# Performance work log

Hardware: AMD Instinct MI355X
Metric: run time of the kernel (lower is better)

## Reference

```python
import jax, jax.numpy as jnp
import numpy as np

B, N, K, DIN, C = 2, 20480, 16, 32, 64  # C = 2*d_out
EPS = 1e-5


def _ln(x, g, b):
    m = jnp.mean(x, axis=-1, keepdims=True)
    v = jnp.mean((x - m) ** 2, axis=-1, keepdims=True)
    return (x - m) * jax.lax.rsqrt(v + EPS) * g + b


def _gather(pc, idx):
    # pc: (B, N, D), idx: (B, N, K) -> (B, N, K, D)
    Bq, Nq, Kq = idx.shape
    D = pc.shape[-1]
    flat = idx.reshape(Bq, Nq * Kq, 1)
    return jnp.take_along_axis(pc, flat, axis=1).reshape(Bq, Nq, Kq, D)


def setup_inputs() -> dict:
    key = jax.random.key(0)
    ks = jax.random.split(key, 40)
    rn = lambda k, s, sc=0.05: jax.random.normal(k, s, dtype=jnp.float32) * sc
    inp = {
        "feature": rn(ks[0], (B, DIN, N, 1), 1.0),
        "xyz": jax.random.uniform(ks[1], (B, N, 3), dtype=jnp.float32),
        "W1": rn(ks[2], (C, DIN)), "b1": rn(ks[3], (C,)),
        "Wq": rn(ks[4], (C, C)), "bq": rn(ks[5], (C,)),
        "Wk": rn(ks[6], (C, C)), "bk": rn(ks[7], (C,)),
        "Wv": rn(ks[8], (C, C)), "bv": rn(ks[9], (C,)),
        "Wd1": rn(ks[10], (3, 3), 0.3), "bd1": rn(ks[11], (3,)),
        "lnd1_g": 1.0 + rn(ks[12], (3,)), "lnd1_b": rn(ks[13], (3,)),
        "Wd2": rn(ks[14], (C, 3), 0.3), "bd2": rn(ks[15], (C,)),
        "Wg1": rn(ks[16], (C, C)), "bg1": rn(ks[17], (C,)),
        "lng1_g": 1.0 + rn(ks[18], (C,)), "lng1_b": rn(ks[19], (C,)),
        "Wg2": rn(ks[20], (C, C)), "bg2": rn(ks[21], (C,)),
        "lng2_g": 1.0 + rn(ks[22], (C,)), "lng2_b": rn(ks[23], (C,)),
        "Wmlp": rn(ks[24], (C, C)),
        "bnm_g": 1.0 + rn(ks[25], (C,)), "bnm_b": rn(ks[26], (C,)),
        "bnm_m": rn(ks[27], (C,)), "bnm_v": 1.0 + jax.random.uniform(ks[28], (C,), dtype=jnp.float32) * 0.1,
        "Wsc": rn(ks[29], (C, DIN)),
        "bns_g": 1.0 + rn(ks[30], (C,)), "bns_b": rn(ks[31], (C,)),
        "bns_m": rn(ks[32], (C,)), "bns_v": 1.0 + jax.random.uniform(ks[33], (C,), dtype=jnp.float32) * 0.1,
        "neigh_idx": jax.random.randint(ks[34], (B, N, K), 0, N),
    }
    return inp


def reference(feature, xyz, W1, b1, Wq, bq, Wk, bk, Wv, bv, Wd1, bd1, lnd1_g, lnd1_b,
              Wd2, bd2, Wg1, bg1, lng1_g, lng1_b, Wg2, bg2, lng2_g, lng2_b,
              Wmlp, bnm_g, bnm_b, bnm_m, bnm_v, Wsc, bns_g, bns_b, bns_m, bns_v,
              neigh_idx):
    f = jnp.transpose(feature[..., 0], (0, 2, 1))          # (B, N, DIN)
    x = f @ W1.T + b1                                      # (B, N, C)
    q = x @ Wq.T + bq                                      # (B, N, C)
    kf = _gather(x @ Wk.T + bk, neigh_idx)                 # (B, N, K, C)
    vf = _gather(x @ Wv.T + bv, neigh_idx)                 # (B, N, K, C)
    knn_xyz = _gather(xyz, neigh_idx)                      # (B, N, K, 3)
    rel = xyz[:, :, None, :] - knn_xyz                     # (B, N, K, 3)
    pos = rel @ Wd1.T + bd1
    pos = jax.nn.relu(_ln(pos, lnd1_g, lnd1_b))
    pos = pos @ Wd2.T + bd2                                # (B, N, K, C)
    attn = q[:, :, None, :] - kf + pos
    attn = jax.nn.relu(_ln(attn, lng1_g, lng1_b)) @ Wg1.T + bg1
    attn = jax.nn.relu(_ln(attn, lng2_g, lng2_b)) @ Wg2.T + bg2
    attn = jax.nn.softmax(attn, axis=2)                    # softmax over K
    res = jnp.sum(attn * (vf + pos), axis=2)               # (B, N, C)
    # mlp: 1x1 conv (no bias) + BN(eval) + ReLU
    res = res @ Wmlp.T
    res = jax.nn.relu(bnm_g * (res - bnm_m) * jax.lax.rsqrt(bnm_v + EPS) + bnm_b)
    # shortcut: 1x1 conv (no bias) + BN(eval) + ReLU
    sc = f @ Wsc.T
    sc = jax.nn.relu(bns_g * (sc - bns_m) * jax.lax.rsqrt(bns_v + EPS) + bns_b)
    out = jax.nn.leaky_relu(res + sc, negative_slope=0.2)  # (B, N, C)
    return jnp.transpose(out, (0, 2, 1))[..., None]        # (B, C, N, 1)
```

## Files before the change

### kernel.cpp

```cpp
#include <hip/hip_runtime.h>

#define N_ 20480
#define EPS_ 1e-5f

typedef __bf16 bf16;
typedef __attribute__((ext_vector_type(8))) __bf16 bf16x8;
typedef __attribute__((ext_vector_type(4))) float f32x4;
typedef __attribute__((ext_vector_type(2))) float f32x2;

#define WS_WG1   0
#define WS_WG2   8192
#define WS_PCST  16384
#define WS_L1    17408
#define WS_L2    17920
#define WS_BG1   18432
#define WS_BG2   18688
#define WS_WQ    18944
#define WS_WK    23040
#define WS_WV    27136
#define WS_WSC   31232
#define WS_WMLP  35328
#define WS_BQ    43520
#define WS_BK    43776
#define WS_BV    44032
#define WS_BSC   44288
#define WS_BMLP  44544
#define WS_PD1   44800
#define WS_FLAG  44872
#define WS_PREP  45056

template <typename T>
__device__ __forceinline__ float ldf(const T* p, size_t i) { return (float)p[i]; }

__global__ void detect_dtype(const unsigned int* __restrict__ xyz_raw, int* __restrict__ flag) {
  __shared__ int cnt[256];
  int t = threadIdx.x;
  int local = 0;
  for (int i = t; i < 4096; i += 256) {
    unsigned int wv = xyz_raw[i];
    unsigned int b1 = (wv >> 8) & 0xFFu;
    local += (b1 >= 0x30u && b1 < 0x45u) ? 1 : 0;
  }
  cnt[t] = local;
  __syncthreads();
  for (int s = 128; s > 0; s >>= 1) {
    if (t < s) cnt[t] += cnt[t + s];
    __syncthreads();
  }
  if (t == 0) flag[0] = (cnt[0] > 2048) ? 1 : 0;
}

template <typename T>
__device__ void prep_body(const T* W1, const T* b1, const T* Wq, const T* bq,
                          const T* Wk, const T* bk, const T* Wv, const T* bv,
                          const T* Wd1, const T* bd1, const T* lnd1_g, const T* lnd1_b,
                          const T* Wd2, const T* bd2,
                          const T* Wg1, const T* bg1, const T* lng1_g, const T* lng1_b,
                          const T* Wg2, const T* bg2, const T* lng2_g, const T* lng2_b,
                          const T* Wmlp, const T* bnm_g, const T* bnm_b, const T* bnm_m, const T* bnm_v,
                          const T* Wsc, const T* bns_g, const T* bns_b, const T* bns_m, const T* bns_v,
                          char* wsp) {
  const int t = threadIdx.x;
  bf16* wg1bf = (bf16*)(wsp + WS_WG1);
  bf16* wg2bf = (bf16*)(wsp + WS_WG2);
  bf16* wmlpbf = (bf16*)(wsp + WS_WMLP);
  bf16* wscbf = (bf16*)(wsp + WS_WSC);
  bf16* wqbf = (bf16*)(wsp + WS_WQ);
  bf16* wkbf = (bf16*)(wsp + WS_WK);
  bf16* wvbf = (bf16*)(wsp + WS_WV);
  float* pcst = (float*)(wsp + WS_PCST);
  float* l1c = (float*)(wsp + WS_L1);
  float* l2c = (float*)(wsp + WS_L2);
  float* bg1f = (float*)(wsp + WS_BG1);
  float* bg2f = (float*)(wsp + WS_BG2);
  float* bqf = (float*)(wsp + WS_BQ);
  float* bkf = (float*)(wsp + WS_BK);
  float* bvf = (float*)(wsp + WS_BV);
  float* bscf = (float*)(wsp + WS_BSC);
  float* bmlpf = (float*)(wsp + WS_BMLP);
  float* pd1 = (float*)(wsp + WS_PD1);

  for (int i = t; i < 4096; i += 256) {
    wg1bf[i] = (__bf16)ldf(Wg1, i);
    wg2bf[i] = (__bf16)ldf(Wg2, i);
    int c = i >> 6;
    float s = ldf(bnm_g, c) * rsqrtf(ldf(bnm_v, c) + EPS_);
    wmlpbf[i] = (__bf16)(s * ldf(Wmlp, i));
  }
  for (int i = t; i < 2048; i += 256) {
    int c = i >> 5;
    float s = ldf(bns_g, c) * rsqrtf(ldf(bns_v, c) + EPS_);
    wscbf[i] = (__bf16)(s * ldf(Wsc, i));
  }
  for (int o = t; o < 2048; o += 256) {
    int c = o >> 5, d = o & 31;
    float aq = 0.f, ak = 0.f, av = 0.f;
    for (int cc = 0; cc < 64; ++cc) {
      float w1v = ldf(W1, cc * 32 + d);
      aq = fmaf(ldf(Wq, c * 64 + cc), w1v, aq);
      ak = fmaf(ldf(Wk, c * 64 + cc), w1v, ak);
      av = fmaf(ldf(Wv, c * 64 + cc), w1v, av);
    }
    wqbf[o] = (__bf16)aq; wkbf[o] = (__bf16)ak; wvbf[o] = (__bf16)av;
  }
  if (t < 64) {
    pcst[t * 4 + 0] = ldf(Wd2, t * 3 + 0);
    pcst[t * 4 + 1] = ldf(Wd2, t * 3 + 1);
    pcst[t * 4 + 2] = ldf(Wd2, t * 3 + 2);
    pcst[t * 4 + 3] = ldf(bd2, t);
    l1c[t * 2 + 0] = ldf(lng1_g, t); l1c[t * 2 + 1] = ldf(lng1_b, t);
    l2c[t * 2 + 0] = ldf(lng2_g, t); l2c[t * 2 + 1] = ldf(lng2_b, t);
    bg1f[t] = ldf(bg1, t); bg2f[t] = ldf(bg2, t);
    float aq = ldf(bq, t), ak = ldf(bk, t), av = ldf(bv, t);
    for (int cc = 0; cc < 64; ++cc) {
      float b1v = ldf(b1, cc);
      aq = fmaf(ldf(Wq, t * 64 + cc), b1v, aq);
      ak = fmaf(ldf(Wk, t * 64 + cc), b1v, ak);
      av = fmaf(ldf(Wv, t * 64 + cc), b1v, av);
    }
    bqf[t] = aq; bkf[t] = ak; bvf[t] = av;
    float sm = ldf(bnm_g, t) * rsqrtf(ldf(bnm_v, t) + EPS_);
    bmlpf[t] = ldf(bnm_b, t) - ldf(bnm_m, t) * sm;
    float ss = ldf(bns_g, t) * rsqrtf(ldf(bns_v, t) + EPS_);
    bscf[t] = ldf(bns_b, t) - ldf(bns_m, t) * ss;
  }
  if (t < 9) pd1[t] = ldf(Wd1, t);
  if (t < 3) {
    pd1[9 + t] = ldf(bd1, t);
    pd1[12 + t] = ldf(lnd1_g, t);
    pd1[15 + t] = ldf(lnd1_b, t);
  }
}

__launch_bounds__(256)
__global__ void prep_kernel(const void* W1, const void* b1, const void* Wq, const void* bq,
                            const void* Wk, const void* bk, const void* Wv, const void* bv,
                            const void* Wd1, const void* bd1, const void* lnd1_g, const void* lnd1_b,
                            const void* Wd2, const void* bd2,
                            const void* Wg1, const void* bg1, const void* lng1_g, const void* lng1_b,
                            const void* Wg2, const void* bg2, const void* lng2_g, const void* lng2_b,
                            const void* Wmlp, const void* bnm_g, const void* bnm_b, const void* bnm_m,
                            const void* bnm_v, const void* Wsc, const void* bns_g, const void* bns_b,
                            const void* bns_m, const void* bns_v, char* wsp) {
  const int* flag = (const int*)(wsp + WS_FLAG);
  if (flag[0])
    prep_body<bf16>((const bf16*)W1, (const bf16*)b1, (const bf16*)Wq, (const bf16*)bq,
                    (const bf16*)Wk, (const bf16*)bk, (const bf16*)Wv, (const bf16*)bv,
                    (const bf16*)Wd1, (const bf16*)bd1, (const bf16*)lnd1_g, (const bf16*)lnd1_b,
                    (const bf16*)Wd2, (const bf16*)bd2,
                    (const bf16*)Wg1, (const bf16*)bg1, (const bf16*)lng1_g, (const bf16*)lng1_b,
                    (const bf16*)Wg2, (const bf16*)bg2, (const bf16*)lng2_g, (const bf16*)lng2_b,
                    (const bf16*)Wmlp, (const bf16*)bnm_g, (const bf16*)bnm_b, (const bf16*)bnm_m,
                    (const bf16*)bnm_v, (const bf16*)Wsc, (const bf16*)bns_g, (const bf16*)bns_b,
                    (const bf16*)bns_m, (const bf16*)bns_v, wsp);
  else
    prep_body<float>((const float*)W1, (const float*)b1, (const float*)Wq, (const float*)bq,
                     (const float*)Wk, (const float*)bk, (const float*)Wv, (const float*)bv,
                     (const float*)Wd1, (const float*)bd1, (const float*)lnd1_g, (const float*)lnd1_b,
                     (const float*)Wd2, (const float*)bd2,
                     (const float*)Wg1, (const float*)bg1, (const float*)lng1_g, (const float*)lng1_b,
                     (const float*)Wg2, (const float*)bg2, (const float*)lng2_g, (const float*)lng2_b,
                     (const float*)Wmlp, (const float*)bnm_g, (const float*)bnm_b, (const float*)bnm_m,
                     (const float*)bnm_v, (const float*)Wsc, (const float*)bns_g, (const float*)bns_b,
                     (const float*)bns_m, (const float*)bns_v, wsp);
}

template <typename T>
__device__ void xqkv_body(const T* feat, const char* wsp,
                          bf16* q_ws, bf16* k_ws, bf16* v_ws, float (*tile)[68]) {
  const int t = threadIdx.x, w = t >> 6, lane = t & 63;
  const int m = lane & 15, g = lane >> 4;
  const int p0 = blockIdx.x * 64 + w * 16;
  const int b = p0 / N_, n0 = p0 % N_;
  const bf16* wqbf = (const bf16*)(wsp + WS_WQ);
  const bf16* wkbf = (const bf16*)(wsp + WS_WK);
  const bf16* wvbf = (const bf16*)(wsp + WS_WV);
  const float* bqf = (const float*)(wsp + WS_BQ);
  const float* bkf = (const float*)(wsp + WS_BK);
  const float* bvf = (const float*)(wsp + WS_BV);
  float (*tw)[68] = tile + w * 16;

  bf16x8 fa;
  #pragma unroll
  for (int j = 0; j < 8; ++j)
    fa[j] = (__bf16)ldf(feat, ((size_t)b * 32 + g * 8 + j) * N_ + n0 + m);

  auto matmul16 = [&](const bf16* wbf, const float* bias, float* ob) {
    #pragma unroll
    for (int tt = 0; tt < 4; ++tt) {
      bf16x8 wf = *(const bf16x8*)(wbf + (tt * 16 + m) * 32 + g * 8);
      float bb = bias[tt * 16 + m];
      f32x4 ci = {bb, bb, bb, bb};
      ci = __builtin_amdgcn_mfma_f32_16x16x32_bf16(fa, wf, ci, 0, 0, 0);
      #pragma unroll
      for (int r = 0; r < 4; ++r) tw[g * 4 + r][tt * 16 + m] = ci[r];
    }
    #pragma unroll
    for (int s = 0; s < 2; ++s) {
      f32x4 v0 = *(f32x4*)&tw[m][s * 32 + g * 8];
      f32x4 v1 = *(f32x4*)&tw[m][s * 32 + g * 8 + 4];
      #pragma unroll
      for (int r = 0; r < 4; ++r) { ob[s * 8 + r] = v0[r]; ob[s * 8 + 4 + r] = v1[r]; }
    }
  };
  float ob[16];
  bf16x8 o0, o1;
  matmul16(wqbf, bqf, ob);
  #pragma unroll
  for (int j = 0; j < 8; ++j) { o0[j] = (__bf16)ob[j]; o1[j] = (__bf16)ob[8 + j]; }
  *(bf16x8*)(q_ws + (size_t)(p0 + m) * 64 + g * 8) = o0;
  *(bf16x8*)(q_ws + (size_t)(p0 + m) * 64 + 32 + g * 8) = o1;
  matmul16(wkbf, bkf, ob);
  #pragma unroll
  for (int j = 0; j < 8; ++j) { o0[j] = (__bf16)ob[j]; o1[j] = (__bf16)ob[8 + j]; }
  *(bf16x8*)(k_ws + (size_t)(p0 + m) * 64 + g * 8) = o0;
  *(bf16x8*)(k_ws + (size_t)(p0 + m) * 64 + 32 + g * 8) = o1;
  matmul16(wvbf, bvf, ob);
  #pragma unroll
  for (int j = 0; j < 8; ++j) { o0[j] = (__bf16)ob[j]; o1[j] = (__bf16)ob[8 + j]; }
  *(bf16x8*)(v_ws + (size_t)(p0 + m) * 64 + g * 8) = o0;
  *(bf16x8*)(v_ws + (size_t)(p0 + m) * 64 + 32 + g * 8) = o1;
}

__launch_bounds__(256)
__global__ void xqkv_kernel(const void* feat, char* wsp,
                            bf16* q_ws, bf16* k_ws, bf16* v_ws) {
  __shared__ float tile[64][68];
  const int* flag = (const int*)(wsp + WS_FLAG);
  if (flag[0]) xqkv_body<bf16>((const bf16*)feat, wsp, q_ws, k_ws, v_ws, tile);
  else         xqkv_body<float>((const float*)feat, wsp, q_ws, k_ws, v_ws, tile);
}

template <typename T>
__device__ void attn_body(const T* xyz, const int* nidx, const char* wsp,
                          bf16* qres, const bf16* k_ws, const bf16* v_ws,
                          f32x4* pcstL, f32x2* l1L, f32x2* l2L,
                          float (*vpf)[68], float (*scr)[68]) {
  const int t = threadIdx.x;
  ((float*)pcstL)[t] = ((const float*)(wsp + WS_PCST))[t];
  if (t < 128) ((float*)l1L)[t] = ((const float*)(wsp + WS_L1))[t];
  else if (t < 256) ((float*)l2L)[t - 128] = ((const float*)(wsp + WS_L2))[t - 128];
  __syncthreads();

  const int w = t >> 6, lane = t & 63, m = lane & 15, g = lane >> 4;
  const int p = blockIdx.x * 4 + w;
  const int b = p / N_;
  float (*vw)[68] = vpf + w * 16;
  float (*sw)[68] = scr + w * 16;

  const float* pd1 = (const float*)(wsp + WS_PD1);
  const float* bg1f = (const float*)(wsp + WS_BG1);
  const float* bg2f = (const float*)(wsp + WS_BG2);
  const bf16* wg1bf = (const bf16*)(wsp + WS_WG1);
  const bf16* wg2bf = (const bf16*)(wsp + WS_WG2);

  float bg1r[4], bg2r[4];
  #pragma unroll
  for (int tt = 0; tt < 4; ++tt) { bg1r[tt] = bg1f[tt * 16 + m]; bg2r[tt] = bg2f[tt * 16 + m]; }

  float xp = ldf(xyz, (size_t)p * 3 + 0);
  float yp = ldf(xyz, (size_t)p * 3 + 1);
  float zp = ldf(xyz, (size_t)p * 3 + 2);

  int idx = nidx[(size_t)p * 16 + m];
  size_t pg = (size_t)b * N_ + idx;
  bf16x8 kf0 = *(const bf16x8*)(k_ws + pg * 64 + g * 8);
  bf16x8 kf1 = *(const bf16x8*)(k_ws + pg * 64 + 32 + g * 8);
  bf16x8 vf0 = *(const bf16x8*)(v_ws + pg * 64 + g * 8);
  bf16x8 vf1 = *(const bf16x8*)(v_ws + pg * 64 + 32 + g * 8);
  bf16x8 qf0 = *(const bf16x8*)(qres + (size_t)p * 64 + g * 8);
  bf16x8 qf1 = *(const bf16x8*)(qres + (size_t)p * 64 + 32 + g * 8);
  float nx = ldf(xyz, pg * 3 + 0), ny = ldf(xyz, pg * 3 + 1), nz = ldf(xyz, pg * 3 + 2);

  float rx = xp - nx, ry = yp - ny, rz = zp - nz;
  float pp0 = pd1[0] * rx + pd1[1] * ry + pd1[2] * rz + pd1[9];
  float pp1 = pd1[3] * rx + pd1[4] * ry + pd1[5] * rz + pd1[10];
  float pp2 = pd1[6] * rx + pd1[7] * ry + pd1[8] * rz + pd1[11];
  float mu3 = (pp0 + pp1 + pp2) * (1.f / 3.f);
  float q0 = pp0 - mu3, q1 = pp1 - mu3, q2 = pp2 - mu3;
  float vr3 = (q0 * q0 + q1 * q1 + q2 * q2) * (1.f / 3.f);
  float rs3 = rsqrtf(vr3 + EPS_);
  float h0 = fmaxf(q0 * rs3 * pd1[12] + pd1[15], 0.f);
  float h1 = fmaxf(q1 * rs3 * pd1[13] + pd1[16], 0.f);
  float h2 = fmaxf(q2 * rs3 * pd1[14] + pd1[17], 0.f);

  float a[16];
  #pragma unroll
  for (int s = 0; s < 2; ++s)
    #pragma unroll
    for (int half = 0; half < 2; ++half) {
      f32x4 vout;
      #pragma unroll
      for (int q4 = 0; q4 < 4; ++q4) {
        int j = half * 4 + q4;
        int c = s * 32 + g * 8 + j;
        f32x4 pc = pcstL[c];
        float pos = fmaf(h0, pc[0], fmaf(h1, pc[1], fmaf(h2, pc[2], pc[3])));
        float kv = (float)((s == 0) ? kf0[j] : kf1[j]);
        float vv = (float)((s == 0) ? vf0[j] : vf1[j]);
        float qv = (float)((s == 0) ? qf0[j] : qf1[j]);
        vout[q4] = vv + pos;
        a[s * 8 + j] = qv - kv + pos;
      }
      *(f32x4*)&vw[m][s * 32 + g * 8 + half * 4] = vout;
    }

  f32x4 acc[4];
  bf16x8 hf0, hf1;

  {
    float s1 = 0.f, s2 = 0.f;
    #pragma unroll
    for (int i = 0; i < 16; ++i) { s1 += a[i]; s2 = fmaf(a[i], a[i], s2); }
    s1 += __shfl_xor(s1, 16); s2 += __shfl_xor(s2, 16);
    s1 += __shfl_xor(s1, 32); s2 += __shfl_xor(s2, 32);
    float mean = s1 * (1.f / 64.f);
    float var = s2 * (1.f / 64.f) - mean * mean;
    float rsv = rsqrtf(var + EPS_);
    #pragma unroll
    for (int s = 0; s < 2; ++s)
      #pragma unroll
      for (int j = 0; j < 8; ++j) {
        int c = s * 32 + g * 8 + j;
        f32x2 lc = l1L[c];
        float hh = fmaxf(fmaf((a[s * 8 + j] - mean) * rsv, lc[0], lc[1]), 0.f);
        if (s == 0) hf0[j] = (__bf16)hh; else hf1[j] = (__bf16)hh;
      }
  }
  #pragma unroll
  for (int tt = 0; tt < 4; ++tt) {
    bf16x8 w0 = *(const bf16x8*)(wg1bf + (tt * 16 + m) * 64 + g * 8);
    bf16x8 w1 = *(const bf16x8*)(wg1bf + (tt * 16 + m) * 64 + 32 + g * 8);
    f32x4 ci = {bg1r[tt], bg1r[tt], bg1r[tt], bg1r[tt]};
    ci = __builtin_amdgcn_mfma_f32_16x16x32_bf16(hf0, w0, ci, 0, 0, 0);
    ci = __builtin_amdgcn_mfma_f32_16x16x32_bf16(hf1, w1, ci, 0, 0, 0);
    acc[tt] = ci;
  }
  #pragma unroll
  for (int tt = 0; tt < 4; ++tt)
    #pragma unroll
    for (int r = 0; r < 4; ++r)
      sw[g * 4 + r][tt * 16 + m] = acc[tt][r];
  #pragma unroll
  for (int s = 0; s < 2; ++s) {
    f32x4 v0 = *(f32x4*)&sw[m][s * 32 + g * 8];
    f32x4 v1 = *(f32x4*)&sw[m][s * 32 + g * 8 + 4];
    #pragma unroll
    for (int r = 0; r < 4; ++r) { a[s * 8 + r] = v0[r]; a[s * 8 + 4 + r] = v1[r]; }
  }
  {
    float s1 = 0.f, s2 = 0.f;
    #pragma unroll
    for (int i = 0; i < 16; ++i) { s1 += a[i]; s2 = fmaf(a[i], a[i], s2); }
    s1 += __shfl_xor(s1, 16); s2 += __shfl_xor(s2, 16);
    s1 += __shfl_xor(s1, 32); s2 += __shfl_xor(s2, 32);
    float mean = s1 * (1.f / 64.f);
    float var = s2 * (1.f / 64.f) - mean * mean;
    float rsv = rsqrtf(var + EPS_);
    #pragma unroll
    for (int s = 0; s < 2; ++s)
      #pragma unroll
      for (int j = 0; j < 8; ++j) {
        int c = s * 32 + g * 8 + j;
        f32x2 lc = l2L[c];
        float hh = fmaxf(fmaf((a[s * 8 + j] - mean) * rsv, lc[0], lc[1]), 0.f);
        if (s == 0) hf0[j] = (__bf16)hh; else hf1[j] = (__bf16)hh;
      }
  }
  #pragma unroll
  for (int tt = 0; tt < 4; ++tt) {
    bf16x8 w0 = *(const bf16x8*)(wg2bf + (tt * 16 + m) * 64 + g * 8);
    bf16x8 w1 = *(const bf16x8*)(wg2bf + (tt * 16 + m) * 64 + 32 + g * 8);
    f32x4 ci = {bg2r[tt], bg2r[tt], bg2r[tt], bg2r[tt]};
    ci = __builtin_amdgcn_mfma_f32_16x16x32_bf16(hf0, w0, ci, 0, 0, 0);
    ci = __builtin_amdgcn_mfma_f32_16x16x32_bf16(hf1, w1, ci, 0, 0, 0);
    acc[tt] = ci;
  }
  float resv[4];
  #pragma unroll
  for (int tt = 0; tt < 4; ++tt) {
    f32x4 l = acc[tt];
    float mx = fmaxf(fmaxf(l[0], l[1]), fmaxf(l[2], l[3]));
    mx = fmaxf(mx, __shfl_xor(mx, 16));
    mx = fmaxf(mx, __shfl_xor(mx, 32));
    float x0 = __expf(l[0] - mx), x1 = __expf(l[1] - mx);
    float x2 = __expf(l[2] - mx), x3 = __expf(l[3] - mx);
    float ss = x0 + x1 + x2 + x3;
    ss += __shfl_xor(ss, 16); ss += __shfl_xor(ss, 32);
    int cc = tt * 16 + m;
    float part = x0 * vw[g * 4 + 0][cc] + x1 * vw[g * 4 + 1][cc]
               + x2 * vw[g * 4 + 2][cc] + x3 * vw[g * 4 + 3][cc];
    part += __shfl_xor(part, 16); part += __shfl_xor(part, 32);
    resv[tt] = part / ss;
  }
  float outv = (g == 0) ? resv[0] : (g == 1) ? resv[1] : (g == 2) ? resv[2] : resv[3];
  qres[(size_t)p * 64 + lane] = (__bf16)outv;
}

__launch_bounds__(256)
__global__ void attn_kernel(const void* xyz, const int* __restrict__ nidx, char* wsp,
                            bf16* qres, const bf16* k_ws, const bf16* v_ws) {
  __shared__ f32x4 pcstL[64];
  __shared__ f32x2 l1L[64];
  __shared__ f32x2 l2L[64];
  __shared__ float vpf[64][68];
  __shared__ float scr[64][68];
  const int* flag = (const int*)(wsp + WS_FLAG);
  if (flag[0])
    attn_body<bf16>((const bf16*)xyz, nidx, wsp, qres, k_ws, v_ws, pcstL, l1L, l2L, vpf, scr);
  else
    attn_body<float>((const float*)xyz, nidx, wsp, qres, k_ws, v_ws, pcstL, l1L, l2L, vpf, scr);
}

template <typename T>
__device__ void out_body(const T* feat, const bf16* res_ws, const char* wsp, T* out,
                         float (*tileT)[68]) {
  const int t = threadIdx.x, w = t >> 6, lane = t & 63;
  const int m = lane & 15, g = lane >> 4;
  const int p0blk = blockIdx.x * 64;
  const int b = p0blk / N_, n0 = p0blk % N_;
  const int p0w = p0blk + w * 16;
  const bf16* wmlpbf = (const bf16*)(wsp + WS_WMLP);
  const bf16* wscbf = (const bf16*)(wsp + WS_WSC);
  const float* bmlpf = (const float*)(wsp + WS_BMLP);
  const float* bscf = (const float*)(wsp + WS_BSC);

  bf16x8 ar0 = *(const bf16x8*)(res_ws + (size_t)(p0w + m) * 64 + g * 8);
  bf16x8 ar1 = *(const bf16x8*)(res_ws + (size_t)(p0w + m) * 64 + 32 + g * 8);
  bf16x8 af;
  #pragma unroll
  for (int j = 0; j < 8; ++j)
    af[j] = (__bf16)ldf(feat, ((size_t)b * 32 + g * 8 + j) * N_ + (n0 + w * 16) + m);

  #pragma unroll
  for (int tt = 0; tt < 4; ++tt) {
    bf16x8 wm0 = *(const bf16x8*)(wmlpbf + (tt * 16 + m) * 64 + g * 8);
    bf16x8 wm1 = *(const bf16x8*)(wmlpbf + (tt * 16 + m) * 64 + 32 + g * 8);
    bf16x8 wsf = *(const bf16x8*)(wscbf + (tt * 16 + m) * 32 + g * 8);
    float bm = bmlpf[tt * 16 + m], bs = bscf[tt * 16 + m];
    f32x4 cm = {bm, bm, bm, bm};
    cm = __builtin_amdgcn_mfma_f32_16x16x32_bf16(ar0, wm0, cm, 0, 0, 0);
    cm = __builtin_amdgcn_mfma_f32_16x16x32_bf16(ar1, wm1, cm, 0, 0, 0);
    f32x4 cs = {bs, bs, bs, bs};
    cs = __builtin_amdgcn_mfma_f32_16x16x32_bf16(af, wsf, cs, 0, 0, 0);
    #pragma unroll
    for (int r = 0; r < 4; ++r) {
      float o = fmaxf(cm[r], 0.f) + fmaxf(cs[r], 0.f);
      o = (o > 0.f) ? o : 0.2f * o;
      tileT[tt * 16 + m][w * 16 + g * 4 + r] = o;
    }
  }
  __syncthreads();
  const int ln = t & 63, grp = t >> 6;
  #pragma unroll
  for (int k = 0; k < 16; ++k) {
    int c2 = grp * 16 + k;
    out[((size_t)b * 64 + c2) * N_ + n0 + ln] = (T)tileT[c2][ln];
  }
}

__launch_bounds__(256)
__global__ void out_kernel(const void* feat, const bf16* res_ws, char* wsp, void* out) {
  __shared__ float tileT[64][68];
  const int* flag = (const int*)(wsp + WS_FLAG);
  if (flag[0]) out_body<bf16>((const bf16*)feat, res_ws, wsp, (bf16*)out, tileT);
  else         out_body<float>((const float*)feat, res_ws, wsp, (float*)out, tileT);
}

extern "C" void kernel_launch(void* const* d_in, const int* in_sizes, int n_in,
                              void* d_out, int out_size, void* d_ws, size_t ws_size,
                              hipStream_t stream) {
  const void* feature = d_in[0];
  const void* xyz     = d_in[1];
  const int*  nidx    = (const int*)d_in[34];

  char* ws = (char*)d_ws;
  bf16* q_ws = (bf16*)(ws + WS_PREP);
  bf16* k_ws = (bf16*)(ws + WS_PREP + 5242880);
  bf16* v_ws = (bf16*)(ws + WS_PREP + 10485760);

  detect_dtype<<<1, 256, 0, stream>>>((const unsigned int*)xyz, (int*)(ws + WS_FLAG));
  prep_kernel<<<1, 256, 0, stream>>>(d_in[2], d_in[3], d_in[4], d_in[5], d_in[6], d_in[7],
                                     d_in[8], d_in[9], d_in[10], d_in[11], d_in[12], d_in[13],
                                     d_in[14], d_in[15], d_in[16], d_in[17], d_in[18], d_in[19],
                                     d_in[20], d_in[21], d_in[22], d_in[23], d_in[24], d_in[25],
                                     d_in[26], d_in[27], d_in[28], d_in[29], d_in[30], d_in[31],
                                     d_in[32], d_in[33], ws);
  xqkv_kernel<<<640, 256, 0, stream>>>(feature, ws, q_ws, k_ws, v_ws);
  attn_kernel<<<10240, 256, 0, stream>>>(xyz, nidx, ws, q_ws, k_ws, v_ws);
  out_kernel<<<640, 256, 0, stream>>>(feature, q_ws, ws, d_out);
}
```

Measured before the change: 293.9 us.

## Store attention LDS scratch in bf16, raise occupancy hint, parallelize prep kernel

```diff
diff --git a/kernel.cpp b/kernel.cpp
--- a/kernel.cpp
+++ b/kernel.cpp
@@ -5,6 +5,7 @@
 
 typedef __bf16 bf16;
 typedef __attribute__((ext_vector_type(8))) __bf16 bf16x8;
+typedef __attribute__((ext_vector_type(4))) __bf16 bf16x4;
 typedef __attribute__((ext_vector_type(4))) float f32x4;
 typedef __attribute__((ext_vector_type(2))) float f32x2;
 
@@ -60,7 +61,8 @@
                           const T* Wmlp, const T* bnm_g, const T* bnm_b, const T* bnm_m, const T* bnm_v,
                           const T* Wsc, const T* bns_g, const T* bns_b, const T* bns_m, const T* bns_v,
                           char* wsp) {
-  const int t = threadIdx.x;
+  const int tid = blockIdx.x * 256 + threadIdx.x;
+  const int T_ = gridDim.x * 256;
   bf16* wg1bf = (bf16*)(wsp + WS_WG1);
   bf16* wg2bf = (bf16*)(wsp + WS_WG2);
   bf16* wmlpbf = (bf16*)(wsp + WS_WMLP);
@@ -80,19 +82,19 @@
   float* bmlpf = (float*)(wsp + WS_BMLP);
   float* pd1 = (float*)(wsp + WS_PD1);
 
-  for (int i = t; i < 4096; i += 256) {
+  for (int i = tid; i < 4096; i += T_) {
     wg1bf[i] = (__bf16)ldf(Wg1, i);
     wg2bf[i] = (__bf16)ldf(Wg2, i);
     int c = i >> 6;
     float s = ldf(bnm_g, c) * rsqrtf(ldf(bnm_v, c) + EPS_);
     wmlpbf[i] = (__bf16)(s * ldf(Wmlp, i));
   }
-  for (int i = t; i < 2048; i += 256) {
+  for (int i = tid; i < 2048; i += T_) {
     int c = i >> 5;
     float s = ldf(bns_g, c) * rsqrtf(ldf(bns_v, c) + EPS_);
     wscbf[i] = (__bf16)(s * ldf(Wsc, i));
   }
-  for (int o = t; o < 2048; o += 256) {
+  for (int o = tid; o < 2048; o += T_) {
     int c = o >> 5, d = o & 31;
     float aq = 0.f, ak = 0.f, av = 0.f;
     for (int cc = 0; cc < 64; ++cc) {
@@ -103,7 +105,8 @@
     }
     wqbf[o] = (__bf16)aq; wkbf[o] = (__bf16)ak; wvbf[o] = (__bf16)av;
   }
-  if (t < 64) {
+  if (tid < 64) {
+    int t = tid;
     pcst[t * 4 + 0] = ldf(Wd2, t * 3 + 0);
     pcst[t * 4 + 1] = ldf(Wd2, t * 3 + 1);
     pcst[t * 4 + 2] = ldf(Wd2, t * 3 + 2);
@@ -124,11 +127,12 @@
     float ss = ldf(bns_g, t) * rsqrtf(ldf(bns_v, t) + EPS_);
     bscf[t] = ldf(bns_b, t) - ldf(bns_m, t) * ss;
   }
-  if (t < 9) pd1[t] = ldf(Wd1, t);
-  if (t < 3) {
-    pd1[9 + t] = ldf(bd1, t);
-    pd1[12 + t] = ldf(lnd1_g, t);
-    pd1[15 + t] = ldf(lnd1_b, t);
+  if (tid >= 64 && tid < 64 + 9) pd1[tid - 64] = ldf(Wd1, tid - 64);
+  if (tid >= 80 && tid < 83) {
+    int i = tid - 80;
+    pd1[9 + i] = ldf(bd1, i);
+    pd1[12 + i] = ldf(lnd1_g, i);
+    pd1[15 + i] = ldf(lnd1_b, i);
   }
 }
 
@@ -235,7 +239,7 @@
 __device__ void attn_body(const T* xyz, const int* nidx, const char* wsp,
                           bf16* qres, const bf16* k_ws, const bf16* v_ws,
                           f32x4* pcstL, f32x2* l1L, f32x2* l2L,
-                          float (*vpf)[68], float (*scr)[68]) {
+                          bf16 (*vpf)[72], bf16 (*scr)[72]) {
   const int t = threadIdx.x;
   ((float*)pcstL)[t] = ((const float*)(wsp + WS_PCST))[t];
   if (t < 128) ((float*)l1L)[t] = ((const float*)(wsp + WS_L1))[t];
@@ -245,8 +249,8 @@
   const int w = t >> 6, lane = t & 63, m = lane & 15, g = lane >> 4;
   const int p = blockIdx.x * 4 + w;
   const int b = p / N_;
-  float (*vw)[68] = vpf + w * 16;
-  float (*sw)[68] = scr + w * 16;
+  bf16 (*vw)[72] = vpf + w * 16;
+  bf16 (*sw)[72] = scr + w * 16;
 
   const float* pd1 = (const float*)(wsp + WS_PD1);
   const float* bg1f = (const float*)(wsp + WS_BG1);
@@ -289,7 +293,7 @@
   for (int s = 0; s < 2; ++s)
     #pragma unroll
     for (int half = 0; half < 2; ++half) {
-      f32x4 vout;
+      bf16x4 vb;
       #pragma unroll
       for (int q4 = 0; q4 < 4; ++q4) {
         int j = half * 4 + q4;
@@ -299,10 +303,10 @@
         float kv = (float)((s == 0) ? kf0[j] : kf1[j]);
         float vv = (float)((s == 0) ? vf0[j] : vf1[j]);
         float qv = (float)((s == 0) ? qf0[j] : qf1[j]);
-        vout[q4] = vv + pos;
+        vb[q4] = (__bf16)(vv + pos);
         a[s * 8 + j] = qv - kv + pos;
       }
-      *(f32x4*)&vw[m][s * 32 + g * 8 + half * 4] = vout;
+      *(bf16x4*)&vw[m][s * 32 + g * 8 + half * 4] = vb;
     }
 
   f32x4 acc[4];
@@ -340,13 +344,12 @@
   for (int tt = 0; tt < 4; ++tt)
     #pragma unroll
     for (int r = 0; r < 4; ++r)
-      sw[g * 4 + r][tt * 16 + m] = acc[tt][r];
+      sw[g * 4 + r][tt * 16 + m] = (__bf16)acc[tt][r];
   #pragma unroll
   for (int s = 0; s < 2; ++s) {
-    f32x4 v0 = *(f32x4*)&sw[m][s * 32 + g * 8];
-    f32x4 v1 = *(f32x4*)&sw[m][s * 32 + g * 8 + 4];
-    #pragma unroll
-    for (int r = 0; r < 4; ++r) { a[s * 8 + r] = v0[r]; a[s * 8 + 4 + r] = v1[r]; }
+    bf16x8 av = *(bf16x8*)&sw[m][s * 32 + g * 8];
+    #pragma unroll
+    for (int j = 0; j < 8; ++j) a[s * 8 + j] = (float)av[j];
   }
   {
     float s1 = 0.f, s2 = 0.f;
@@ -388,8 +391,8 @@
     float ss = x0 + x1 + x2 + x3;
     ss += __shfl_xor(ss, 16); ss += __shfl_xor(ss, 32);
     int cc = tt * 16 + m;
-    float part = x0 * vw[g * 4 + 0][cc] + x1 * vw[g * 4 + 1][cc]
-               + x2 * vw[g * 4 + 2][cc] + x3 * vw[g * 4 + 3][cc];
+    float part = x0 * (float)vw[g * 4 + 0][cc] + x1 * (float)vw[g * 4 + 1][cc]
+               + x2 * (float)vw[g * 4 + 2][cc] + x3 * (float)vw[g * 4 + 3][cc];
     part += __shfl_xor(part, 16); part += __shfl_xor(part, 32);
     resv[tt] = part / ss;
   }
@@ -397,14 +400,14 @@
   qres[(size_t)p * 64 + lane] = (__bf16)outv;
 }
 
-__launch_bounds__(256)
+__launch_bounds__(256, 8)
 __global__ void attn_kernel(const void* xyz, const int* __restrict__ nidx, char* wsp,
                             bf16* qres, const bf16* k_ws, const bf16* v_ws) {
   __shared__ f32x4 pcstL[64];
   __shared__ f32x2 l1L[64];
   __shared__ f32x2 l2L[64];
-  __shared__ float vpf[64][68];
-  __shared__ float scr[64][68];
+  __shared__ bf16 vpf[64][72];
+  __shared__ bf16 scr[64][72];
   const int* flag = (const int*)(wsp + WS_FLAG);
   if (flag[0])
     attn_body<bf16>((const bf16*)xyz, nidx, wsp, qres, k_ws, v_ws, pcstL, l1L, l2L, vpf, scr);
@@ -480,12 +483,12 @@
   bf16* v_ws = (bf16*)(ws + WS_PREP + 10485760);
 
   detect_dtype<<<1, 256, 0, stream>>>((const unsigned int*)xyz, (int*)(ws + WS_FLAG));
-  prep_kernel<<<1, 256, 0, stream>>>(d_in[2], d_in[3], d_in[4], d_in[5], d_in[6], d_in[7],
-                                     d_in[8], d_in[9], d_in[10], d_in[11], d_in[12], d_in[13],
-                                     d_in[14], d_in[15], d_in[16], d_in[17], d_in[18], d_in[19],
-                                     d_in[20], d_in[21], d_in[22], d_in[23], d_in[24], d_in[25],
-                                     d_in[26], d_in[27], d_in[28], d_in[29], d_in[30], d_in[31],
-                                     d_in[32], d_in[33], ws);
+  prep_kernel<<<64, 256, 0, stream>>>(d_in[2], d_in[3], d_in[4], d_in[5], d_in[6], d_in[7],
+                                      d_in[8], d_in[9], d_in[10], d_in[11], d_in[12], d_in[13],
+                                      d_in[14], d_in[15], d_in[16], d_in[17], d_in[18], d_in[19],
+                                      d_in[20], d_in[21], d_in[22], d_in[23], d_in[24], d_in[25],
+                                      d_in[26], d_in[27], d_in[28], d_in[29], d_in[30], d_in[31],
+                                      d_in[32], d_in[33], ws);
   xqkv_kernel<<<640, 256, 0, stream>>>(feature, ws, q_ws, k_ws, v_ws);
   attn_kernel<<<10240, 256, 0, stream>>>(xyz, nidx, ws, q_ws, k_ws, v_ws);
   out_kernel<<<640, 256, 0, stream>>>(feature, q_ws, ws, d_out);
```

Result: no change. 291.6 us (-0.8%).
